# Performance work log

Hardware: AMD Instinct MI355X
Metric: run time of the kernel (lower is better)

## Reference

```python
import jax, jax.numpy as jnp
import numpy as np

EPS = 1e-5
HEADS = 2


def _batch_norm(x, gamma, beta, axes):
    # Training-mode batch norm (biased variance), channel axis = 1.
    m = jnp.mean(x, axes, keepdims=True)
    v = jnp.mean((x - m) ** 2, axes, keepdims=True)
    shape = [1] * x.ndim
    shape[1] = x.shape[1]
    return (x - m) * jax.lax.rsqrt(v + EPS) * gamma.reshape(shape) + beta.reshape(shape)


def setup_inputs() -> dict:
    key = jax.random.key(0)
    ks = jax.random.split(key, 6)
    b, n, H, W = 64, 2, 32, 32
    dim = H * W            # 1024
    inner = dim * HEADS    # 2048
    s = 0.02
    return {
        "x": jax.random.normal(ks[0], (b, n, H, W), jnp.float32),
        "Wq": jax.random.normal(ks[1], (inner, dim), jnp.float32) * s,
        "Wk": jax.random.normal(ks[2], (inner, dim), jnp.float32) * s,
        "Wv": jax.random.normal(ks[3], (inner, dim), jnp.float32) * s,
        "Wo": jax.random.normal(ks[4], (dim, inner), jnp.float32) * s,
        "bo": jnp.zeros((dim,), jnp.float32),
        "g_q": jnp.ones((2,), jnp.float32), "b_q": jnp.zeros((2,), jnp.float32),
        "g_k": jnp.ones((2,), jnp.float32), "b_k": jnp.zeros((2,), jnp.float32),
        "g_v": jnp.ones((2,), jnp.float32), "b_v": jnp.zeros((2,), jnp.float32),
        "g_bn": jnp.ones((2,), jnp.float32), "b_bn": jnp.zeros((2,), jnp.float32),
    }


def reference(x, Wq, Wk, Wv, Wo, bo, g_q, b_q, g_k, b_k, g_v, b_v, g_bn, b_bn):
    b, n, H, W = x.shape
    h = HEADS
    dim = H * W
    xf = x.reshape(b, n, dim)

    # to_q/to_k/to_v: Linear (no bias) + BatchNorm1d over channel dim n=2
    q = _batch_norm(xf @ Wq.T, g_q, b_q, (0, 2))  # (b, n, h*dim)
    k = _batch_norm(xf @ Wk.T, g_k, b_k, (0, 2))
    v = _batch_norm(xf @ Wv.T, g_v, b_v, (0, 2))

    def split_heads(t):  # b n (h d) -> b h n d
        return t.reshape(b, n, h, dim).transpose(0, 2, 1, 3)

    q, k, v = split_heads(q), split_heads(k), split_heads(v)

    # linear (kernelized) attention
    k_cumsum = k.sum(axis=-2)                                   # (b, h, d)
    D_inv = 1.0 / jnp.einsum('bhnd,bhd->bhn', q, k_cumsum)      # (b, h, n)
    context = jnp.einsum('bhnd,bhne->bhde', k, v)               # (b, h, d, d)
    out = jnp.einsum('bhde,bhnd,bhn->bhne', context, q, D_inv)  # (b, h, n, d)

    out = out.transpose(0, 2, 1, 3).reshape(b, n, h * dim)      # b h n d -> b n (h d)
    out = out @ Wo.T + bo                                       # to_out
    out = out.reshape(b, n, H, W)                               # dropout p=0 is identity
    return _batch_norm(out, g_bn, b_bn, (0, 2, 3))              # BatchNorm2d(2)
```

## Files before the change

### kernel.cpp

```cpp
#include <hip/hip_runtime.h>
#include <stdint.h>

typedef __bf16 bf16x8 __attribute__((ext_vector_type(8)));
typedef float f32x4 __attribute__((ext_vector_type(4)));

#define EPS 1e-5f

#define OFF_SQ    0
#define OFF_Q     4096
#define OFF_AHI   (OFF_Q + 3145728)
#define OFF_SO    (OFF_AHI + 524288)
#define OFF_PROJ  (OFF_SO + 4096)

static __device__ __forceinline__ unsigned short f2b(float f) {
  return __builtin_bit_cast(unsigned short, (__bf16)f);
}

__device__ __forceinline__ float wave_red(float v) {
#pragma unroll
  for (int o = 32; o > 0; o >>= 1) v += __shfl_down(v, o);
  return v;
}

#define GLDS16(g, l)                                             \
  __builtin_amdgcn_global_load_lds(                              \
      (const __attribute__((address_space(1))) void*)(g),        \
      (__attribute__((address_space(3))) void*)(l), 16, 0, 0)

static __device__ __forceinline__ void frag_split(const float* base, int c0, int s,
                                                  bf16x8& hi, bf16x8& lo) {
  int q0 = c0 ^ s;
  float4 v0 = *(const float4*)(base + q0 * 4);
  float4 v1 = *(const float4*)(base + (q0 ^ 1) * 4);
  float a[8] = {v0.x, v0.y, v0.z, v0.w, v1.x, v1.y, v1.z, v1.w};
#pragma unroll
  for (int i = 0; i < 8; ++i) {
    __bf16 h = (__bf16)a[i];
    hi[i] = h;
    lo[i] = (__bf16)(a[i] - (float)h);
  }
}
static __device__ __forceinline__ bf16x8 frag_cvt(const float* base, int c0, int s) {
  int q0 = c0 ^ s;
  float4 v0 = *(const float4*)(base + q0 * 4);
  float4 v1 = *(const float4*)(base + (q0 ^ 1) * 4);
  bf16x8 r;
  r[0] = (__bf16)v0.x; r[1] = (__bf16)v0.y; r[2] = (__bf16)v0.z; r[3] = (__bf16)v0.w;
  r[4] = (__bf16)v1.x; r[5] = (__bf16)v1.y; r[6] = (__bf16)v1.z; r[7] = (__bf16)v1.w;
  return r;
}

__global__ __launch_bounds__(256) void qkv_gemm(const float* __restrict__ x,
                                                const float* __restrict__ Wq,
                                                const float* __restrict__ Wk,
                                                const float* __restrict__ Wv,
                                                float* __restrict__ qkv,
                                                float* __restrict__ sq) {
  __shared__ alignas(16) float Af[3][128 * 64];
  __shared__ alignas(16) float Bf[3][32 * 64];
  __shared__ float red[16];

  int mat = blockIdx.x >> 6;
  int nt  = blockIdx.x & 63;
  const float* W = (mat == 0) ? Wq : ((mat == 1) ? Wk : Wv);
  float* outp = qkv + mat * 262144;

  int tid = threadIdx.x, w = tid >> 6, lane = tid & 63;
  int rsel = lane >> 4, ch = lane & 15, l15 = lane & 15;

#define STAGE_Q(c, tt) do {                                                   \
    _Pragma("unroll")                                                         \
    for (int j = 0; j < 8; ++j) {                                             \
      int rl = w * 32 + j * 4 + rsel;                                         \
      GLDS16(x + rl * 1024 + (tt) * 64 + ((ch ^ (rl & 7)) << 2),              \
             &Af[c][(w * 32 + j * 4) * 64]);                                  \
    }                                                                         \
    _Pragma("unroll")                                                         \
    for (int j = 0; j < 2; ++j) {                                             \
      int rl = w * 8 + j * 4 + rsel;                                          \
      GLDS16(W + (nt * 32 + rl) * 1024 + (tt) * 64 +                          \
                 ((ch ^ (rl & 7)) << 2),                                      \
             &Bf[c][(w * 8 + j * 4) * 64]);                                   \
    }                                                                         \
  } while (0)

  f32x4 acc[2][2];
#pragma unroll
  for (int m = 0; m < 2; ++m)
#pragma unroll
    for (int n = 0; n < 2; ++n) acc[m][n] = (f32x4){0.f, 0.f, 0.f, 0.f};

  STAGE_Q(0, 0);
  STAGE_Q(1, 1);
  __syncthreads();

#pragma unroll
  for (int t = 0; t < 16; ++t) {
    const int c = t % 3;
    bf16x8 fah[2][2], fal[2][2], fbh[2][2], fbl[2][2];
#pragma unroll
    for (int ks = 0; ks < 2; ++ks) {
      int kc = ks * 4 + rsel;
#pragma unroll
      for (int m = 0; m < 2; ++m) {
        int ra = w * 32 + m * 16 + l15;
        frag_split(&Af[c][ra * 64], kc * 2, ra & 7, fah[ks][m], fal[ks][m]);
      }
#pragma unroll
      for (int n = 0; n < 2; ++n) {
        int rb = n * 16 + l15;
        frag_split(&Bf[c][rb * 64], kc * 2, rb & 7, fbh[ks][n], fbl[ks][n]);
      }
    }
    if (t < 14) { STAGE_Q((t + 2) % 3, t + 2); }
#pragma unroll
    for (int ks = 0; ks < 2; ++ks)
#pragma unroll
      for (int m = 0; m < 2; ++m)
#pragma unroll
        for (int n = 0; n < 2; ++n) {
          acc[m][n] = __builtin_amdgcn_mfma_f32_16x16x32_bf16(fah[ks][m], fbh[ks][n], acc[m][n], 0, 0, 0);
          acc[m][n] = __builtin_amdgcn_mfma_f32_16x16x32_bf16(fah[ks][m], fbl[ks][n], acc[m][n], 0, 0, 0);
          acc[m][n] = __builtin_amdgcn_mfma_f32_16x16x32_bf16(fal[ks][m], fbh[ks][n], acc[m][n], 0, 0, 0);
        }
    if (t < 15) {
      if (t < 14) { asm volatile("s_waitcnt vmcnt(10) lgkmcnt(0)" ::: "memory"); }
      else        { asm volatile("s_waitcnt vmcnt(0) lgkmcnt(0)" ::: "memory"); }
      __builtin_amdgcn_sched_barrier(0);
      __builtin_amdgcn_s_barrier();
      __builtin_amdgcn_sched_barrier(0);
    }
  }
#undef STAGE_Q

  float s0 = 0, q0 = 0, s1 = 0, q1 = 0;
#pragma unroll
  for (int m = 0; m < 2; ++m)
#pragma unroll
    for (int n = 0; n < 2; ++n)
#pragma unroll
      for (int r = 0; r < 4; ++r) {
        int row = w * 32 + m * 16 + (lane >> 4) * 4 + r;
        int col = nt * 32 + n * 16 + l15;
        float v = acc[m][n][r];
        outp[row * 2048 + col] = v;
        if (r & 1) { s1 += v; q1 += v * v; } else { s0 += v; q0 += v * v; }
      }
  s0 = wave_red(s0); q0 = wave_red(q0); s1 = wave_red(s1); q1 = wave_red(q1);
  if (lane == 0) { red[w * 4 + 0] = s0; red[w * 4 + 1] = q0; red[w * 4 + 2] = s1; red[w * 4 + 3] = q1; }
  __syncthreads();
  if (tid == 0) {
    float a0 = 0, a1 = 0, a2 = 0, a3 = 0;
    for (int i = 0; i < 4; ++i) { a0 += red[i * 4 + 0]; a1 += red[i * 4 + 1]; a2 += red[i * 4 + 2]; a3 += red[i * 4 + 3]; }
    *(float4*)(sq + blockIdx.x * 4) = (float4){a0, a1, a2, a3};
  }
}

__global__ __launch_bounds__(256) void attn_kernel(const float* __restrict__ qkv,
                                                   const float* __restrict__ sq,
                                                   ushort* __restrict__ ahi,
                                                   const float* __restrict__ g_q, const float* __restrict__ b_q,
                                                   const float* __restrict__ g_k, const float* __restrict__ b_k,
                                                   const float* __restrict__ g_v, const float* __restrict__ b_v) {
  __shared__ float sm[12];
  __shared__ float red[16];
  __shared__ float bc[4];
  int bh = blockIdx.x, b = bh >> 1, h = bh & 1;
  int tid = threadIdx.x, w = tid >> 6, lane = tid & 63;

  if (tid < 192) {
    float4 p = *(const float4*)(sq + tid * 4);
    float a0 = wave_red(p.x), a1 = wave_red(p.y), a2 = wave_red(p.z), a3 = wave_red(p.w);
    if (lane == 0) { sm[w * 4 + 0] = a0; sm[w * 4 + 1] = a1; sm[w * 4 + 2] = a2; sm[w * 4 + 3] = a3; }
  }
  __syncthreads();

  const float cnt = 131072.f;
  float qs[2], qo[2], kc_[2], ko[2], vs[2], vo[2];
#pragma unroll
  for (int c = 0; c < 2; ++c) {
    float m, var, inv;
    m = sm[0 + 2 * c] / cnt; var = sm[1 + 2 * c] / cnt - m * m; inv = rsqrtf(var + EPS);
    qs[c] = g_q[c] * inv; qo[c] = b_q[c] - m * qs[c];
    m = sm[4 + 2 * c] / cnt; var = sm[5 + 2 * c] / cnt - m * m; inv = rsqrtf(var + EPS);
    kc_[c] = g_k[c] * inv; ko[c] = b_k[c] - m * kc_[c];
    m = sm[8 + 2 * c] / cnt; var = sm[9 + 2 * c] / cnt - m * m; inv = rsqrtf(var + EPS);
    vs[c] = g_v[c] * inv; vo[c] = b_v[c] - m * vs[c];
  }

  const float* Q = qkv;
  const float* K = qkv + 262144;
  const float* V = qkv + 524288;
  const float* q0p = Q + (b * 2 + 0) * 2048 + h * 1024;
  const float* q1p = Q + (b * 2 + 1) * 2048 + h * 1024;
  const float* k0p = K + (b * 2 + 0) * 2048 + h * 1024;
  const float* k1p = K + (b * 2 + 1) * 2048 + h * 1024;
  const float* v0p = V + (b * 2 + 0) * 2048 + h * 1024;
  const float* v1p = V + (b * 2 + 1) * 2048 + h * 1024;

  float p00 = 0, p01 = 0, p10 = 0, p11 = 0;
#pragma unroll
  for (int i = 0; i < 4; ++i) {
    int d = tid + i * 256;
    float a0 = q0p[d] * qs[0] + qo[0];
    float a1 = q1p[d] * qs[1] + qo[1];
    float c0 = k0p[d] * kc_[0] + ko[0];
    float c1 = k1p[d] * kc_[1] + ko[1];
    p00 += a0 * c0; p01 += a0 * c1; p10 += a1 * c0; p11 += a1 * c1;
  }
  p00 = wave_red(p00); p01 = wave_red(p01); p10 = wave_red(p10); p11 = wave_red(p11);
  if (lane == 0) { red[w * 4 + 0] = p00; red[w * 4 + 1] = p01; red[w * 4 + 2] = p10; red[w * 4 + 3] = p11; }
  __syncthreads();
  if (tid < 4) bc[tid] = red[0 + tid] + red[4 + tid] + red[8 + tid] + red[12 + tid];
  __syncthreads();
  float s00 = bc[0], s01 = bc[1], s10 = bc[2], s11 = bc[3];
  float di0 = 1.f / (s00 + s01), di1 = 1.f / (s10 + s11);
  int o0 = (b * 2 + 0) * 2048 + h * 1024;
  int o1 = (b * 2 + 1) * 2048 + h * 1024;
#pragma unroll
  for (int i = 0; i < 4; ++i) {
    int d = tid + i * 256;
    float v0 = v0p[d] * vs[0] + vo[0];
    float v1 = v1p[d] * vs[1] + vo[1];
    ahi[o0 + d] = f2b((s00 * v0 + s01 * v1) * di0);
    ahi[o1 + d] = f2b((s10 * v0 + s11 * v1) * di1);
  }
}

__global__ __launch_bounds__(256) void out_gemm(const ushort* __restrict__ ahi,
                                                const float* __restrict__ Wo,
                                                const float* __restrict__ bo,
                                                float* __restrict__ proj,
                                                float* __restrict__ so) {
  __shared__ alignas(16) ushort Ab[3][64 * 128];
  __shared__ alignas(16) float  Bf[3][16 * 128];
  __shared__ float red[16];

  int mt = blockIdx.x >> 6;
  int nt = blockIdx.x & 63;

  int tid = threadIdx.x, w = tid >> 6, lane = tid & 63;
  int rsel4 = lane >> 4, ch16 = lane & 15;
  int rsel2 = lane >> 5, ch32 = lane & 31;

#define STAGE_O(c, tt) do {                                                   \
    _Pragma("unroll")                                                         \
    for (int j = 0; j < 4; ++j) {                                             \
      int rl = w * 16 + j * 4 + rsel4;                                        \
      GLDS16(ahi + (mt * 64 + rl) * 2048 + (tt) * 128 +                       \
                 ((ch16 ^ (rl & 7)) << 3),                                    \
             &Ab[c][(w * 16 + j * 4) * 128]);                                 \
    }                                                                         \
    _Pragma("unroll")                                                         \
    for (int j = 0; j < 2; ++j) {                                             \
      int rl = w * 4 + j * 2 + rsel2;                                         \
      GLDS16(Wo + (nt * 16 + rl) * 2048 + (tt) * 128 +                        \
                 ((ch32 ^ (rl & 7)) << 2),                                    \
             &Bf[c][(w * 4 + j * 2) * 128]);                                  \
    }                                                                         \
  } while (0)

  f32x4 acc = (f32x4){0.f, 0.f, 0.f, 0.f};

  STAGE_O(0, 0);
  STAGE_O(1, 1);
  __syncthreads();

#pragma unroll
  for (int t = 0; t < 16; ++t) {
    const int c = t % 3;
    bf16x8 fa[4], fb[4];
#pragma unroll
    for (int ks = 0; ks < 4; ++ks) {
      int kc = ks * 4 + rsel4;
      int ra = w * 16 + (lane & 15);
      fa[ks] = *(const bf16x8*)(&Ab[c][ra * 128 + ((kc ^ (ra & 7)) << 3)]);
      int rb = lane & 15;
      fb[ks] = frag_cvt(&Bf[c][rb * 128], kc * 2, rb & 7);
    }
    if (t < 14) { STAGE_O((t + 2) % 3, t + 2); }
#pragma unroll
    for (int ks = 0; ks < 4; ++ks)
      acc = __builtin_amdgcn_mfma_f32_16x16x32_bf16(fa[ks], fb[ks], acc, 0, 0, 0);
    if (t < 15) {
      if (t < 14) { asm volatile("s_waitcnt vmcnt(6) lgkmcnt(0)" ::: "memory"); }
      else        { asm volatile("s_waitcnt vmcnt(0) lgkmcnt(0)" ::: "memory"); }
      __builtin_amdgcn_sched_barrier(0);
      __builtin_amdgcn_s_barrier();
      __builtin_amdgcn_sched_barrier(0);
    }
  }
#undef STAGE_O

  int col = nt * 16 + (lane & 15);
  float bov = bo[col];
  float s0 = 0, q0 = 0, s1 = 0, q1 = 0;
#pragma unroll
  for (int r = 0; r < 4; ++r) {
    int grow = mt * 64 + w * 16 + (lane >> 4) * 4 + r;
    float v = acc[r] + bov;
    proj[grow * 1024 + col] = v;
    if (r & 1) { s1 += v; q1 += v * v; } else { s0 += v; q0 += v * v; }
  }
  s0 = wave_red(s0); q0 = wave_red(q0); s1 = wave_red(s1); q1 = wave_red(q1);
  if (lane == 0) { red[w * 4 + 0] = s0; red[w * 4 + 1] = q0; red[w * 4 + 2] = s1; red[w * 4 + 3] = q1; }
  __syncthreads();
  if (tid == 0) {
    float a0 = 0, a1 = 0, a2 = 0, a3 = 0;
    for (int i = 0; i < 4; ++i) { a0 += red[i * 4 + 0]; a1 += red[i * 4 + 1]; a2 += red[i * 4 + 2]; a3 += red[i * 4 + 3]; }
    *(float4*)(so + blockIdx.x * 4) = (float4){a0, a1, a2, a3};
  }
}

__global__ __launch_bounds__(256) void final_kernel(const float* __restrict__ proj,
                                                    const float* __restrict__ so,
                                                    const float* __restrict__ g_bn,
                                                    const float* __restrict__ b_bn,
                                                    float* __restrict__ out) {
  __shared__ float sm[8];
  int tid = threadIdx.x, w = tid >> 6;
  int r = blockIdx.x;
  if (tid < 128) {
    float4 p = *(const float4*)(so + tid * 4);
    float a0 = wave_red(p.x), a1 = wave_red(p.y), a2 = wave_red(p.z), a3 = wave_red(p.w);
    if ((tid & 63) == 0) { sm[w * 4 + 0] = a0; sm[w * 4 + 1] = a1; sm[w * 4 + 2] = a2; sm[w * 4 + 3] = a3; }
  }
  __syncthreads();
  float s0 = sm[0] + sm[4], q0 = sm[1] + sm[5];
  float s1 = sm[2] + sm[6], q1 = sm[3] + sm[7];
  int ch = r & 1;
  float m = (ch ? s1 : s0) / 65536.f;
  float var = (ch ? q1 : q0) / 65536.f - m * m;
  float sc = g_bn[ch] * rsqrtf(var + EPS);
  float sh = b_bn[ch] - m * sc;
  float4 v = *(const float4*)(proj + r * 1024 + tid * 4);
  float4 o = {v.x * sc + sh, v.y * sc + sh, v.z * sc + sh, v.w * sc + sh};
  *(float4*)(out + r * 1024 + tid * 4) = o;
}

extern "C" void kernel_launch(void* const* d_in, const int* in_sizes, int n_in,
                              void* d_out, int out_size, void* d_ws, size_t ws_size,
                              hipStream_t stream) {
  (void)in_sizes; (void)n_in; (void)out_size; (void)ws_size;
  const float* x    = (const float*)d_in[0];
  const float* Wq   = (const float*)d_in[1];
  const float* Wk   = (const float*)d_in[2];
  const float* Wv   = (const float*)d_in[3];
  const float* Wo   = (const float*)d_in[4];
  const float* bo   = (const float*)d_in[5];
  const float* g_q  = (const float*)d_in[6];
  const float* b_q  = (const float*)d_in[7];
  const float* g_k  = (const float*)d_in[8];
  const float* b_k  = (const float*)d_in[9];
  const float* g_v  = (const float*)d_in[10];
  const float* b_v  = (const float*)d_in[11];
  const float* g_bn = (const float*)d_in[12];
  const float* b_bn = (const float*)d_in[13];
  char* ws = (char*)d_ws;
  float* out = (float*)d_out;

  float*  sq   = (float*)(ws + OFF_SQ);
  float*  qkv  = (float*)(ws + OFF_Q);
  ushort* ahi  = (ushort*)(ws + OFF_AHI);
  float*  so   = (float*)(ws + OFF_SO);
  float*  proj = (float*)(ws + OFF_PROJ);

  hipLaunchKernelGGL(qkv_gemm,     dim3(192), dim3(256), 0, stream, x, Wq, Wk, Wv, qkv, sq);
  hipLaunchKernelGGL(attn_kernel,  dim3(128), dim3(256), 0, stream, qkv, sq, ahi,
                     g_q, b_q, g_k, b_k, g_v, b_v);
  hipLaunchKernelGGL(out_gemm,     dim3(128), dim3(256), 0, stream, ahi, Wo, bo, proj, so);
  hipLaunchKernelGGL(final_kernel, dim3(128), dim3(256), 0, stream, proj, so, g_bn, b_bn, out);
}
```

Baseline: 41.09 us.

## Double wave count in QKV GEMM and shrink A staging to double-buffer

The QKV projection GEMM now runs 512 threads (8 waves) per block, each wave owning 16 rows instead of 32, which halves per-wave accumulators and fragment registers. The A tile moves from triple to double buffering with a prefetch distance of one, while B stays triple-buffered, and the waitcnt thresholds are adjusted to match. The aim is more latency hiding and less per-wave register pressure with the same grid of 192 blocks. The shallower A prefetch may expose more global-load latency, and B fragments are now converted redundantly by twice as many waves.

Result: slower. 43.49 us (+5.8%).

```diff
diff --git a/kernel.cpp b/kernel.cpp
--- a/kernel.cpp
+++ b/kernel.cpp
@@ -50,15 +50,15 @@
   return r;
 }
 
-__global__ __launch_bounds__(256) void qkv_gemm(const float* __restrict__ x,
+__global__ __launch_bounds__(512) void qkv_gemm(const float* __restrict__ x,
                                                 const float* __restrict__ Wq,
                                                 const float* __restrict__ Wk,
                                                 const float* __restrict__ Wv,
                                                 float* __restrict__ qkv,
                                                 float* __restrict__ sq) {
-  __shared__ alignas(16) float Af[3][128 * 64];
+  __shared__ alignas(16) float Af[2][128 * 64];
   __shared__ alignas(16) float Bf[3][32 * 64];
-  __shared__ float red[16];
+  __shared__ float red[32];
 
   int mat = blockIdx.x >> 6;
   int nt  = blockIdx.x & 63;
@@ -68,90 +68,86 @@
   int tid = threadIdx.x, w = tid >> 6, lane = tid & 63;
   int rsel = lane >> 4, ch = lane & 15, l15 = lane & 15;
 
-#define STAGE_Q(c, tt) do {                                                   \
+#define STAGE_A(c, tt) do {                                                   \
     _Pragma("unroll")                                                         \
-    for (int j = 0; j < 8; ++j) {                                             \
-      int rl = w * 32 + j * 4 + rsel;                                         \
+    for (int j = 0; j < 4; ++j) {                                             \
+      int rl = w * 16 + j * 4 + rsel;                                         \
       GLDS16(x + rl * 1024 + (tt) * 64 + ((ch ^ (rl & 7)) << 2),              \
-             &Af[c][(w * 32 + j * 4) * 64]);                                  \
-    }                                                                         \
-    _Pragma("unroll")                                                         \
-    for (int j = 0; j < 2; ++j) {                                             \
-      int rl = w * 8 + j * 4 + rsel;                                          \
-      GLDS16(W + (nt * 32 + rl) * 1024 + (tt) * 64 +                          \
-                 ((ch ^ (rl & 7)) << 2),                                      \
-             &Bf[c][(w * 8 + j * 4) * 64]);                                   \
+             &Af[c][(w * 16 + j * 4) * 64]);                                  \
     }                                                                         \
   } while (0)
 
-  f32x4 acc[2][2];
-#pragma unroll
-  for (int m = 0; m < 2; ++m)
-#pragma unroll
-    for (int n = 0; n < 2; ++n) acc[m][n] = (f32x4){0.f, 0.f, 0.f, 0.f};
-
-  STAGE_Q(0, 0);
-  STAGE_Q(1, 1);
-  __syncthreads();
-
+#define STAGE_B(c, tt) do {                                                   \
+    int rl = w * 4 + rsel;                                                    \
+    GLDS16(W + (nt * 32 + rl) * 1024 + (tt) * 64 + ((ch ^ (rl & 7)) << 2),    \
+           &Bf[c][(w * 4) * 64]);                                             \
+  } while (0)
+
+  f32x4 acc[2];
+  acc[0] = (f32x4){0.f, 0.f, 0.f, 0.f};
+  acc[1] = (f32x4){0.f, 0.f, 0.f, 0.f};
+
+  STAGE_A(0, 0);
+  STAGE_B(0, 0);
+  STAGE_B(1, 1);
+  asm volatile("s_waitcnt vmcnt(1) lgkmcnt(0)" ::: "memory");
+  __builtin_amdgcn_sched_barrier(0);
+  __builtin_amdgcn_s_barrier();
+  __builtin_amdgcn_sched_barrier(0);
+
+  const int ra = w * 16 + l15;
 #pragma unroll
   for (int t = 0; t < 16; ++t) {
-    const int c = t % 3;
-    bf16x8 fah[2][2], fal[2][2], fbh[2][2], fbl[2][2];
+    const int cA = t & 1, cB = t % 3;
+    bf16x8 fah[2], fal[2], fbh[2][2], fbl[2][2];
 #pragma unroll
     for (int ks = 0; ks < 2; ++ks) {
       int kc = ks * 4 + rsel;
-#pragma unroll
-      for (int m = 0; m < 2; ++m) {
-        int ra = w * 32 + m * 16 + l15;
-        frag_split(&Af[c][ra * 64], kc * 2, ra & 7, fah[ks][m], fal[ks][m]);
-      }
+      frag_split(&Af[cA][ra * 64], kc * 2, ra & 7, fah[ks], fal[ks]);
 #pragma unroll
       for (int n = 0; n < 2; ++n) {
         int rb = n * 16 + l15;
-        frag_split(&Bf[c][rb * 64], kc * 2, rb & 7, fbh[ks][n], fbl[ks][n]);
+        frag_split(&Bf[cB][rb * 64], kc * 2, rb & 7, fbh[ks][n], fbl[ks][n]);
       }
     }
-    if (t < 14) { STAGE_Q((t + 2) % 3, t + 2); }
+    if (t < 15) { STAGE_A((t + 1) & 1, t + 1); }
+    if (t < 14) { STAGE_B((t + 2) % 3, t + 2); }
 #pragma unroll
     for (int ks = 0; ks < 2; ++ks)
 #pragma unroll
-      for (int m = 0; m < 2; ++m)
-#pragma unroll
-        for (int n = 0; n < 2; ++n) {
-          acc[m][n] = __builtin_amdgcn_mfma_f32_16x16x32_bf16(fah[ks][m], fbh[ks][n], acc[m][n], 0, 0, 0);
-          acc[m][n] = __builtin_amdgcn_mfma_f32_16x16x32_bf16(fah[ks][m], fbl[ks][n], acc[m][n], 0, 0, 0);
-          acc[m][n] = __builtin_amdgcn_mfma_f32_16x16x32_bf16(fal[ks][m], fbh[ks][n], acc[m][n], 0, 0, 0);
-        }
+      for (int n = 0; n < 2; ++n) {
+        acc[n] = __builtin_amdgcn_mfma_f32_16x16x32_bf16(fah[ks], fbh[ks][n], acc[n], 0, 0, 0);
+        acc[n] = __builtin_amdgcn_mfma_f32_16x16x32_bf16(fah[ks], fbl[ks][n], acc[n], 0, 0, 0);
+        acc[n] = __builtin_amdgcn_mfma_f32_16x16x32_bf16(fal[ks], fbh[ks][n], acc[n], 0, 0, 0);
+      }
     if (t < 15) {
-      if (t < 14) { asm volatile("s_waitcnt vmcnt(10) lgkmcnt(0)" ::: "memory"); }
+      if (t < 14) { asm volatile("s_waitcnt vmcnt(1) lgkmcnt(0)" ::: "memory"); }
       else        { asm volatile("s_waitcnt vmcnt(0) lgkmcnt(0)" ::: "memory"); }
       __builtin_amdgcn_sched_barrier(0);
       __builtin_amdgcn_s_barrier();
       __builtin_amdgcn_sched_barrier(0);
     }
   }
-#undef STAGE_Q
+#undef STAGE_A
+#undef STAGE_B
 
   float s0 = 0, q0 = 0, s1 = 0, q1 = 0;
 #pragma unroll
-  for (int m = 0; m < 2; ++m)
-#pragma unroll
-    for (int n = 0; n < 2; ++n)
-#pragma unroll
-      for (int r = 0; r < 4; ++r) {
-        int row = w * 32 + m * 16 + (lane >> 4) * 4 + r;
-        int col = nt * 32 + n * 16 + l15;
-        float v = acc[m][n][r];
-        outp[row * 2048 + col] = v;
-        if (r & 1) { s1 += v; q1 += v * v; } else { s0 += v; q0 += v * v; }
-      }
+  for (int n = 0; n < 2; ++n)
+#pragma unroll
+    for (int r = 0; r < 4; ++r) {
+      int row = w * 16 + rsel * 4 + r;
+      int col = nt * 32 + n * 16 + l15;
+      float v = acc[n][r];
+      outp[row * 2048 + col] = v;
+      if (r & 1) { s1 += v; q1 += v * v; } else { s0 += v; q0 += v * v; }
+    }
   s0 = wave_red(s0); q0 = wave_red(q0); s1 = wave_red(s1); q1 = wave_red(q1);
   if (lane == 0) { red[w * 4 + 0] = s0; red[w * 4 + 1] = q0; red[w * 4 + 2] = s1; red[w * 4 + 3] = q1; }
   __syncthreads();
   if (tid == 0) {
     float a0 = 0, a1 = 0, a2 = 0, a3 = 0;
-    for (int i = 0; i < 4; ++i) { a0 += red[i * 4 + 0]; a1 += red[i * 4 + 1]; a2 += red[i * 4 + 2]; a3 += red[i * 4 + 3]; }
+    for (int i = 0; i < 8; ++i) { a0 += red[i * 4 + 0]; a1 += red[i * 4 + 1]; a2 += red[i * 4 + 2]; a3 += red[i * 4 + 3]; }
     *(float4*)(sq + blockIdx.x * 4) = (float4){a0, a1, a2, a3};
   }
 }
@@ -365,7 +361,7 @@
   float*  so   = (float*)(ws + OFF_SO);
   float*  proj = (float*)(ws + OFF_PROJ);
 
-  hipLaunchKernelGGL(qkv_gemm,     dim3(192), dim3(256), 0, stream, x, Wq, Wk, Wv, qkv, sq);
+  hipLaunchKernelGGL(qkv_gemm,     dim3(192), dim3(512), 0, stream, x, Wq, Wk, Wv, qkv, sq);
   hipLaunchKernelGGL(attn_kernel,  dim3(128), dim3(256), 0, stream, qkv, sq, ahi,
                      g_q, b_q, g_k, b_k, g_v, b_v);
   hipLaunchKernelGGL(out_gemm,     dim3(128), dim3(256), 0, stream, ahi, Wo, bo, proj, so);
```
